# Performance work log

Measured on AMD Instinct MI355X. Metric: run time of the kernel, lower is better.

The kernel has to match this reference:

```python
import jax, jax.numpy as jnp
import numpy as np

EMBED_DIM = 256; N_HEADS = 8; HEAD_DIM = 32; N_PAIRS = 16
POS_DIM = 2; N_LEVELS = 4; NBH = [3, 5, 7, 9]
N_Q = 2048; BATCH = 2; FULL = 128
SPATIAL_THETA = 100.0; LEVEL_THETA = 10.0
LN_EPS = 1e-5


def _grids():
    offs, lvls = [], []
    for l, s in enumerate(NBH):
        ax = np.arange(s)
        g = np.stack(np.meshgrid(ax, ax, indexing='ij'), -1).reshape(-1, 2)
        offs.append(g - (s - 1) // 2)
        lvls.append(np.full(s * s, l))
    return (np.concatenate(offs).astype(np.int32), np.concatenate(lvls).astype(np.int32))

OFFSETS, LEVEL_IDS = _grids()  # [164,2], [164]
K_PER_Q = OFFSETS.shape[0]


def _apply_rope(x, pos, freqs):
    # x: [..., n_heads, n_pairs, 2]; pos: [..., 3]; freqs: [3, n_pairs]
    ang = pos @ freqs                      # [..., n_pairs]
    c = jnp.cos(ang)[..., None, :]         # broadcast over heads
    s = jnp.sin(ang)[..., None, :]
    x1, x2 = x[..., 0], x[..., 1]
    return jnp.stack([x1 * c - x2 * s, x1 * s + x2 * c], axis=-1)


def setup_inputs() -> dict:
    key = jax.random.key(0)
    ks = jax.random.split(key, 8)
    scale = EMBED_DIM ** -0.5
    i = jnp.arange(N_PAIRS, dtype=jnp.float32) / N_PAIRS
    rope_freqs = jnp.stack([SPATIAL_THETA ** -i, SPATIAL_THETA ** -i, LEVEL_THETA ** -i])  # [3,16]
    level_spatial_shapes = jnp.array([[FULL >> l, FULL >> l] for l in range(N_LEVELS)], jnp.int32)
    return {
        'query': jax.random.normal(ks[0], (N_Q, EMBED_DIM), jnp.float32),
        'query_spatial_positions': jax.random.uniform(ks[1], (N_Q, POS_DIM), jnp.float32) * (FULL - 1),
        'stacked_feature_maps': jax.random.normal(ks[2], (BATCH, N_LEVELS, FULL, FULL, EMBED_DIM), jnp.float32) * 0.02,
        'norm_w': jnp.ones((EMBED_DIM,), jnp.float32),
        'norm_b': jnp.zeros((EMBED_DIM,), jnp.float32),
        'q_w': jax.random.normal(ks[3], (EMBED_DIM, EMBED_DIM), jnp.float32) * scale,
        'k_w': jax.random.normal(ks[4], (EMBED_DIM, EMBED_DIM), jnp.float32) * scale,
        'v_w': jax.random.normal(ks[5], (EMBED_DIM, EMBED_DIM), jnp.float32) * scale,
        'out_w': jax.random.normal(ks[6], (EMBED_DIM, EMBED_DIM), jnp.float32) * scale,
        'rope_freqs': rope_freqs,
        'query_batch_offsets': jnp.array([0, N_Q // 2, N_Q], jnp.int32),
        'level_spatial_shapes': level_spatial_shapes,
    }


def reference(query, query_spatial_positions, stacked_feature_maps, norm_w, norm_b,
              q_w, k_w, v_w, out_w, rope_freqs, query_batch_offsets, level_spatial_shapes):
    n_q = query.shape[0]
    residual = query

    # pre-LayerNorm
    mu = query.mean(-1, keepdims=True)
    var = query.var(-1, keepdims=True)
    x = (query - mu) * jax.lax.rsqrt(var + LN_EPS) * norm_w + norm_b

    # query projection + RoPE (spatial dims + level dim; queries sit at max-res level 0)
    q = x @ q_w
    qpos = jnp.concatenate([query_spatial_positions, jnp.zeros((n_q, 1), query.dtype)], -1)  # [n_q,3]
    q_rot = _apply_rope(q.reshape(n_q, N_HEADS, N_PAIRS, 2), qpos, rope_freqs).reshape(n_q, N_HEADS, HEAD_DIM)

    # multilevel neighborhood indices
    shapes_f = level_spatial_shapes.astype(query.dtype)               # [L,2]
    scaling = shapes_f / shapes_f.max(0)                              # [L,2]
    scaled = query_spatial_positions[:, None, :] * scaling[None]      # [n_q,L,2]
    centers = jnp.floor(scaled).astype(jnp.int32)                     # [n_q,L,2]
    lvl = jnp.asarray(LEVEL_IDS)                                      # [K]
    idx = centers[:, lvl, :] + jnp.asarray(OFFSETS)[None]             # [n_q,K,2]
    lsh = level_spatial_shapes[lvl]                                   # [K,2]
    valid = jnp.all((idx >= 0) & (idx < lsh[None]), -1)               # [n_q,K]
    idxc = jnp.clip(idx, 0, lsh[None] - 1)

    # per-query batch ids from offsets
    b = jnp.searchsorted(query_batch_offsets, jnp.arange(n_q, dtype=query_batch_offsets.dtype), side='right') - 1

    # sparse gather of key/value features (unspecified -> zero)
    feats = stacked_feature_maps[b[:, None], lvl[None, :], idxc[..., 0], idxc[..., 1]]  # [n_q,K,E]
    feats = feats * valid[..., None].astype(feats.dtype)

    k = feats @ k_w
    v = feats @ v_w

    # key positions at full scale + level coordinate
    stride = (shapes_f.max(0)[None] / shapes_f)[lvl]                  # [K,2]
    kpos_sp = (idx.astype(query.dtype) + 0.5) * stride[None]          # [n_q,K,2]
    kpos = jnp.concatenate([kpos_sp, jnp.broadcast_to(lvl.astype(query.dtype), (n_q, K_PER_Q))[..., None]], -1)
    k_rot = _apply_rope(k.reshape(n_q, K_PER_Q, N_HEADS, N_PAIRS, 2), kpos, rope_freqs)
    k_rot = k_rot.reshape(n_q, K_PER_Q, N_HEADS, HEAD_DIM)

    # attention over the 164 gathered keys per query
    logits = jnp.einsum('nhd,nkhd->nhk', q_rot, k_rot) / np.sqrt(HEAD_DIM)
    logits = jnp.where(valid[:, None, :], logits, jnp.asarray(-1e9, logits.dtype))
    attn = jax.nn.softmax(logits, axis=-1)
    out = jnp.einsum('nhk,nkhd->nhd', attn, v.reshape(n_q, K_PER_Q, N_HEADS, HEAD_DIM))
    out = out.reshape(n_q, EMBED_DIM) @ out_w
    return out + residual
```

## Files before the change

### kernel.cpp

```cpp
#include <hip/hip_runtime.h>
#include <hip/hip_bf16.h>

typedef unsigned short u16;
typedef short short8 __attribute__((ext_vector_type(8)));
typedef float f32x4 __attribute__((ext_vector_type(4)));

#define ROWS_PER_BATCH 21760
#define TOT_ROWS 43520

__device__ __forceinline__ u16 f2bf(float f){
  unsigned u = __builtin_bit_cast(unsigned, f);
  u += 0x7FFFu + ((u >> 16) & 1u);
  return (u16)(u >> 16);
}
__device__ __forceinline__ float bf2f(u16 h){
  return __builtin_bit_cast(float, ((unsigned)h) << 16);
}
__device__ __forceinline__ float bflo(unsigned u){ return __builtin_bit_cast(float, u << 16); }
__device__ __forceinline__ float bfhi(unsigned u){ return __builtin_bit_cast(float, u & 0xFFFF0000u); }
__device__ __forceinline__ unsigned pk2bf(float a, float b){
  __hip_bfloat162 h = __float22bfloat162_rn(make_float2(a, b));
  union { __hip_bfloat162 h2; unsigned u; } cv; cv.h2 = h; return cv.u;
}

__global__ __launch_bounds__(256) void prep_kernel(
    const float* __restrict__ qw, const float* __restrict__ kw,
    const float* __restrict__ vw, const float* __restrict__ ow,
    const float* __restrict__ q, const float* __restrict__ nw,
    const float* __restrict__ nb,
    u16* __restrict__ wtq, u16* __restrict__ wtk,
    u16* __restrict__ wtv, u16* __restrict__ wto, u16* __restrict__ x){
  const int bx = blockIdx.x;
  const int t = threadIdx.x;
  if (bx < 128){
    int e = bx * 256 + t;
    int which = e >> 13;
    int r = e & 8191;
    int cg = r >> 9;
    int kk = (r >> 6) & 7;
    int lane = r & 63;
    int quad = lane >> 4, mn = lane & 15;
    const float* s = which == 0 ? qw : which == 1 ? kw : which == 2 ? vw : ow;
    u16* d       = which == 0 ? wtq : which == 1 ? wtk : which == 2 ? wtv : wto;
    const float* base = s + (kk * 32 + quad * 8) * 256 + cg * 16 + mn;
    float e8[8];
    #pragma unroll
    for (int j = 0; j < 8; ++j) e8[j] = base[j * 256];
    uint4 o = { pk2bf(e8[0], e8[1]), pk2bf(e8[2], e8[3]),
                pk2bf(e8[4], e8[5]), pk2bf(e8[6], e8[7]) };
    *(uint4*)(d + (size_t)r * 8) = o;
  } else {
    const int row = (bx - 128) * 4 + (t >> 6);
    const int lane = t & 63;
    const float4 v = *(const float4*)(q + (size_t)row * 256 + lane * 4);
    float s1 = v.x + v.y + v.z + v.w;
    float s2 = v.x*v.x + v.y*v.y + v.z*v.z + v.w*v.w;
    #pragma unroll
    for (int o = 32; o > 0; o >>= 1){
      s1 += __shfl_xor(s1, o);
      s2 += __shfl_xor(s2, o);
    }
    float mu = s1 * (1.0f / 256.0f);
    float var = s2 * (1.0f / 256.0f) - mu * mu;
    float rs = rsqrtf(var + 1e-5f);
    const float4 wv = *(const float4*)(nw + lane * 4);
    const float4 bv = *(const float4*)(nb + lane * 4);
    float o0 = (v.x - mu) * rs * wv.x + bv.x;
    float o1 = (v.y - mu) * rs * wv.y + bv.y;
    float o2 = (v.z - mu) * rs * wv.z + bv.z;
    float o3 = (v.w - mu) * rs * wv.w + bv.w;
    uint2 pk = { pk2bf(o0, o1), pk2bf(o2, o3) };
    *(uint2*)(x + (size_t)row * 256 + lane * 4) = pk;
  }
}

__global__ __launch_bounds__(256, 4) void kv_gemm(const float* __restrict__ fm,
        const u16* __restrict__ wtkp, const u16* __restrict__ wtvp,
        const float* __restrict__ rope,
        u16* __restrict__ krot, u16* __restrict__ vmap){
  __shared__ float slab[4][16][66];
  __shared__ unsigned sh_cs[4][16][16];

  const int t = threadIdx.x;
  const int row0 = blockIdx.x * 64;
  const int m = blockIdx.y;
  const u16* wtp = m ? wtvp : wtkp;
  u16* outp = m ? vmap : krot;

  const int b = row0 / ROWS_PER_BATCH;
  const int rr = row0 - b * ROWS_PER_BATCH;
  int l, loff;
  if (rr < 16384)      { l = 0; loff = 0; }
  else if (rr < 20480) { l = 1; loff = 16384; }
  else if (rr < 21504) { l = 2; loff = 20480; }
  else                 { l = 3; loff = 21504; }
  const int logW = 7 - l;
  const int Wm1 = (128 >> l) - 1;
  const int cell0 = rr - loff;
  const float* fmbase = fm + (size_t)(b * 4 + l) * (128 * 128 * 256);

  const int wv = t >> 6;
  const int lane = t & 63;
  const int mn = lane & 15;
  const int quad = lane >> 4;

  short8 af[8];
  {
    int cell = cell0 + wv * 16 + mn;
    int y = cell >> logW, x = cell & Wm1;
    const float* arow = fmbase + (((y << 7) + x) << 8) + quad * 8;
    #pragma unroll
    for (int kk = 0; kk < 8; ++kk){
      float4 a0 = *(const float4*)(arow + kk * 32);
      float4 a1 = *(const float4*)(arow + kk * 32 + 4);
      union { short8 s; uint4 u; } cv;
      cv.u = (uint4){ pk2bf(a0.x, a0.y), pk2bf(a0.z, a0.w),
                      pk2bf(a1.x, a1.y), pk2bf(a1.z, a1.w) };
      af[kk] = cv.s;
    }
  }

  if (m == 0){
    #pragma unroll
    for (int i = 0; i < 4; ++i){
      int id = i * 64 + lane;
      int lr = id >> 4, p = id & 15;
      int cell = cell0 + wv * 16 + lr;
      int i0 = cell >> logW;
      int i1 = cell & Wm1;
      float fs = (float)(1 << l);
      float kx = ((float)i0 + 0.5f) * fs;
      float ky = ((float)i1 + 0.5f) * fs;
      float ang = kx * rope[p] + ky * rope[16 + p] + (float)l * rope[32 + p];
      sh_cs[wv][lr][p] = pk2bf(__cosf(ang), __sinf(ang));
    }
  }

  for (int cs2 = 0; cs2 < 4; ++cs2){
    const u16* wb = wtp + (size_t)((cs2 * 4 * 8) * 64 + lane) * 8;
    short8 bc[4], bn[4];
    #pragma unroll
    for (int tl = 0; tl < 4; ++tl)
      bc[tl] = *(const short8*)(wb + (size_t)(tl * 8) * 64 * 8);
    f32x4 acc[4];
    #pragma unroll
    for (int i = 0; i < 4; ++i) acc[i] = (f32x4){0.f, 0.f, 0.f, 0.f};
    #pragma unroll
    for (int kk = 0; kk < 8; ++kk){
      if (kk < 7){
        #pragma unroll
        for (int tl = 0; tl < 4; ++tl)
          bn[tl] = *(const short8*)(wb + (size_t)(tl * 8 + kk + 1) * 64 * 8);
      }
      #pragma unroll
      for (int tl = 0; tl < 4; ++tl)
        acc[tl] = __builtin_amdgcn_mfma_f32_16x16x32_bf16(af[kk], bc[tl], acc[tl], 0, 0, 0);
      #pragma unroll
      for (int tl = 0; tl < 4; ++tl) bc[tl] = bn[tl];
    }
    #pragma unroll
    for (int tl = 0; tl < 4; ++tl)
      #pragma unroll
      for (int r = 0; r < 4; ++r)
        slab[wv][quad * 4 + r][tl * 16 + mn] = acc[tl][r];
    #pragma unroll
    for (int i = 0; i < 8; ++i){
      int pi = i * 64 + lane;
      int row = pi >> 5;
      int pl = pi & 31;
      float2 kv2 = *(const float2*)&slab[wv][row][pl * 2];
      unsigned o;
      if (m == 0){
        unsigned csn = sh_cs[wv][row][pl & 15];
        float c = bflo(csn), s = bfhi(csn);
        o = pk2bf(kv2.x * c - kv2.y * s, kv2.x * s + kv2.y * c);
      } else {
        o = pk2bf(kv2.x, kv2.y);
      }
      *(unsigned*)(outp + (size_t)(row0 + wv * 16 + row) * 256 + cs2 * 64 + pl * 2) = o;
    }
  }
}

__global__ __launch_bounds__(256) void gemm_xw(const u16* __restrict__ A,
        const u16* __restrict__ wt, const float* __restrict__ resid,
        float* __restrict__ out){
  const int t = threadIdx.x;
  const int row0 = blockIdx.x * 16;
  const int wv = t >> 6;
  const int lane = t & 63;
  const int mn = lane & 15;
  const int quad = lane >> 4;
  const int cg = blockIdx.y * 4 + wv;

  short8 af[8];
  {
    const u16* arow = A + (size_t)(row0 + mn) * 256 + quad * 8;
    #pragma unroll
    for (int kk = 0; kk < 8; ++kk)
      af[kk] = *(const short8*)(arow + kk * 32);
  }
  const u16* wb = wt + (size_t)((cg * 8) * 64 + lane) * 8;
  short8 bc = *(const short8*)wb;
  f32x4 acc = (f32x4){0.f, 0.f, 0.f, 0.f};
  #pragma unroll
  for (int kk = 0; kk < 8; ++kk){
    short8 bn;
    if (kk < 7) bn = *(const short8*)(wb + (size_t)(kk + 1) * 64 * 8);
    acc = __builtin_amdgcn_mfma_f32_16x16x32_bf16(af[kk], bc, acc, 0, 0, 0);
    bc = bn;
  }
  const int col = cg * 16 + mn;
  #pragma unroll
  for (int r = 0; r < 4; ++r){
    int row = row0 + quad * 4 + r;
    float val = acc[r];
    if (resid) val += resid[(size_t)row * 256 + col];
    out[(size_t)row * 256 + col] = val;
  }
}

__global__ __launch_bounds__(256) void attn2(
    const float* __restrict__ qraw, const float* __restrict__ qsp,
    const float* __restrict__ rope, const int* __restrict__ qbo, int nbo,
    const u16* __restrict__ krot, const u16* __restrict__ vmap,
    u16* __restrict__ ao){
  __shared__ float sh_q[8][33];
  __shared__ float sh_lg[8][168];
  __shared__ int   sh_row[176];
  __shared__ float sh_inv[8];
  __shared__ float sh_pv[2][128][2];
  const int t = threadIdx.x;
  const int qi = blockIdx.x;

  int bidx = 0;
  for (int j = 1; j < nbo; ++j) if (qi >= qbo[j]) bidx = j;
  const float p0 = qsp[qi * 2 + 0];
  const float p1 = qsp[qi * 2 + 1];

  {
    float qv = qraw[(size_t)qi * 256 + t];
    int p = (t & 31) >> 1;
    float ang = p0 * rope[p] + p1 * rope[16 + p];
    float c = __cosf(ang), s = __sinf(ang);
    float partner = __shfl_xor(qv, 1);
    float val = (t & 1) ? (partner * s + qv * c) : (qv * c - partner * s);
    sh_q[t >> 5][t & 31] = val * 0.17677669529663687f;
  }

  if (t < 164){
    int l, dy, dx, loff;
    if (t < 9)       { l = 0; int j = t;      dy = j / 3 - 1; dx = j % 3 - 1; loff = 0; }
    else if (t < 34) { l = 1; int j = t - 9;  dy = j / 5 - 2; dx = j % 5 - 2; loff = 16384; }
    else if (t < 83) { l = 2; int j = t - 34; dy = j / 7 - 3; dx = j % 7 - 3; loff = 20480; }
    else             { l = 3; int j = t - 83; dy = j / 9 - 4; dx = j % 9 - 4; loff = 21504; }
    float sc = 1.0f / (float)(1 << l);
    int i0 = (int)floorf(p0 * sc) + dy;
    int i1 = (int)floorf(p1 * sc) + dx;
    int W = 128 >> l;
    sh_row[t] = (i0 < 0 || i0 >= W || i1 < 0 || i1 >= W)
              ? -1 : bidx * ROWS_PER_BATCH + loff + (i0 << (7 - l)) + i1;
  }
  __syncthreads();

  const int h = t & 7;
  const int kbase = t >> 3;
  float qreg[32];
  #pragma unroll
  for (int d = 0; d < 32; ++d) qreg[d] = sh_q[h][d];
  for (int pass = 0; pass < 6; ++pass){
    int kk = pass * 32 + kbase;
    if (kk < 164){
      int row = sh_row[kk];
      float lg = -1e9f;
      if (row >= 0){
        const uint4* kp = (const uint4*)(krot + (size_t)row * 256 + h * 32);
        uint4 A0 = kp[0], A1 = kp[1], A2 = kp[2], A3 = kp[3];
        unsigned uu[16];
        uu[0]=A0.x; uu[1]=A0.y; uu[2]=A0.z; uu[3]=A0.w;
        uu[4]=A1.x; uu[5]=A1.y; uu[6]=A1.z; uu[7]=A1.w;
        uu[8]=A2.x; uu[9]=A2.y; uu[10]=A2.z; uu[11]=A2.w;
        uu[12]=A3.x; uu[13]=A3.y; uu[14]=A3.z; uu[15]=A3.w;
        lg = 0.f;
        #pragma unroll
        for (int j = 0; j < 16; ++j)
          lg += qreg[2*j] * bflo(uu[j]) + qreg[2*j+1] * bfhi(uu[j]);
      }
      sh_lg[h][kk] = lg;
    }
  }
  __syncthreads();

  const int h3 = t >> 5;
  const int l32 = t & 31;
  float mx = -1e30f;
  for (int kk = l32; kk < 164; kk += 32) mx = fmaxf(mx, sh_lg[h3][kk]);
  #pragma unroll
  for (int o = 16; o > 0; o >>= 1) mx = fmaxf(mx, __shfl_xor(mx, o));
  float ssum = 0.f;
  for (int kk = l32; kk < 164; kk += 32){
    float e = __expf(sh_lg[h3][kk] - mx);
    sh_lg[h3][kk] = e;
    ssum += e;
  }
  #pragma unroll
  for (int o = 16; o > 0; o >>= 1) ssum += __shfl_xor(ssum, o);
  if (l32 == 0) sh_inv[h3] = 1.0f / ssum;
  __syncthreads();

  {
    const int half = t >> 7;
    const int d2 = t & 127;
    const int hh = d2 >> 4;
    float a0 = 0.f, a1 = 0.f;
    const int k0 = half * 82;
    #pragma unroll 4
    for (int kk = k0; kk < k0 + 82; ++kk){
      int row = sh_row[kk];
      int rc = row < 0 ? 0 : row;
      unsigned vv = *(const unsigned*)(vmap + (size_t)rc * 256 + d2 * 2);
      float e = sh_lg[hh][kk];
      a0 += e * bflo(vv);
      a1 += e * bfhi(vv);
    }
    sh_pv[half][d2][0] = a0;
    sh_pv[half][d2][1] = a1;
  }
  __syncthreads();
  if (t < 128){
    const int hh = t >> 4;
    float inv = sh_inv[hh];
    float o0 = (sh_pv[0][t][0] + sh_pv[1][t][0]) * inv;
    float o1 = (sh_pv[0][t][1] + sh_pv[1][t][1]) * inv;
    *(unsigned*)(ao + (size_t)qi * 256 + t * 2) = pk2bf(o0, o1);
  }
}

extern "C" void kernel_launch(void* const* d_in, const int* in_sizes, int n_in,
                              void* d_out, int out_size, void* d_ws, size_t ws_size,
                              hipStream_t stream) {
  (void)n_in; (void)out_size; (void)ws_size;
  const float* query  = (const float*)d_in[0];
  const float* qsp    = (const float*)d_in[1];
  const float* fm     = (const float*)d_in[2];
  const float* norm_w = (const float*)d_in[3];
  const float* norm_b = (const float*)d_in[4];
  const float* q_w    = (const float*)d_in[5];
  const float* k_w    = (const float*)d_in[6];
  const float* v_w    = (const float*)d_in[7];
  const float* out_w  = (const float*)d_in[8];
  const float* rope   = (const float*)d_in[9];
  const int*   qbo    = (const int*)d_in[10];
  float* out = (float*)d_out;
  const int n_q = in_sizes[0] / 256;
  const int nbo = in_sizes[10];

  char* p = (char*)d_ws;
  u16* krot = (u16*)p;                       p += (size_t)TOT_ROWS * 256 * 2;
  u16* vmap = (u16*)p;                       p += (size_t)TOT_ROWS * 256 * 2;
  float* qraw = (float*)p;                   p += (size_t)n_q * 256 * 4;
  u16* xbf = (u16*)p;                        p += (size_t)n_q * 256 * 2;
  u16* wtq = (u16*)p;                        p += 65536 * 2;
  u16* wtk = (u16*)p;                        p += 65536 * 2;
  u16* wtv = (u16*)p;                        p += 65536 * 2;
  u16* wto = (u16*)p;
  u16* ao = xbf;

  hipLaunchKernelGGL(prep_kernel, dim3(128 + n_q / 4), dim3(256), 0, stream,
                     q_w, k_w, v_w, out_w, query, norm_w, norm_b,
                     wtq, wtk, wtv, wto, xbf);
  hipLaunchKernelGGL(kv_gemm, dim3(TOT_ROWS / 64, 2), dim3(256), 0, stream,
                     fm, wtk, wtv, rope, krot, vmap);
  hipLaunchKernelGGL(gemm_xw, dim3(n_q / 16, 4), dim3(256), 0, stream,
                     xbf, wtq, (const float*)nullptr, qraw);
  hipLaunchKernelGGL(attn2, dim3(n_q), dim3(256), 0, stream,
                     qraw, qsp, rope, qbo, nbo, krot, vmap, ao);
  hipLaunchKernelGGL(gemm_xw, dim3(n_q / 16, 4), dim3(256), 0, stream,
                     ao, wto, query, out);
}
```

Measured before the change: 281.2 us.

## Load feature tile once for K and V, one wavefront per query in attention

The KV projection now uses single-wavefront blocks of 16 rows, each computing both K and V from one register-resident bf16 A tile. Previously the fp32 feature map was read and converted twice, once per projection. The attention kernel maps one query to one wavefront (four per block), which removes block-wide __syncthreads and the split-half PV reduction. The trade-offs are smaller blocks and longer serial loops per wave, which may hurt latency hiding.

```diff
diff --git a/kernel.cpp b/kernel.cpp
--- a/kernel.cpp
+++ b/kernel.cpp
@@ -74,18 +74,15 @@
   }
 }
 
-__global__ __launch_bounds__(256, 4) void kv_gemm(const float* __restrict__ fm,
+__global__ __launch_bounds__(64, 4) void kv_gemm(const float* __restrict__ fm,
         const u16* __restrict__ wtkp, const u16* __restrict__ wtvp,
         const float* __restrict__ rope,
         u16* __restrict__ krot, u16* __restrict__ vmap){
-  __shared__ float slab[4][16][66];
-  __shared__ unsigned sh_cs[4][16][16];
-
-  const int t = threadIdx.x;
-  const int row0 = blockIdx.x * 64;
-  const int m = blockIdx.y;
-  const u16* wtp = m ? wtvp : wtkp;
-  u16* outp = m ? vmap : krot;
+  __shared__ float slab[16][66];
+  __shared__ unsigned sh_cs[16][16];
+
+  const int lane = threadIdx.x;
+  const int row0 = blockIdx.x * 16;
 
   const int b = row0 / ROWS_PER_BATCH;
   const int rr = row0 - b * ROWS_PER_BATCH;
@@ -99,14 +96,12 @@
   const int cell0 = rr - loff;
   const float* fmbase = fm + (size_t)(b * 4 + l) * (128 * 128 * 256);
 
-  const int wv = t >> 6;
-  const int lane = t & 63;
   const int mn = lane & 15;
   const int quad = lane >> 4;
 
   short8 af[8];
   {
-    int cell = cell0 + wv * 16 + mn;
+    int cell = cell0 + mn;
     int y = cell >> logW, x = cell & Wm1;
     const float* arow = fmbase + (((y << 7) + x) << 8) + quad * 8;
     #pragma unroll
@@ -120,64 +115,66 @@
     }
   }
 
-  if (m == 0){
-    #pragma unroll
-    for (int i = 0; i < 4; ++i){
-      int id = i * 64 + lane;
-      int lr = id >> 4, p = id & 15;
-      int cell = cell0 + wv * 16 + lr;
-      int i0 = cell >> logW;
-      int i1 = cell & Wm1;
-      float fs = (float)(1 << l);
-      float kx = ((float)i0 + 0.5f) * fs;
-      float ky = ((float)i1 + 0.5f) * fs;
-      float ang = kx * rope[p] + ky * rope[16 + p] + (float)l * rope[32 + p];
-      sh_cs[wv][lr][p] = pk2bf(__cosf(ang), __sinf(ang));
-    }
-  }
-
-  for (int cs2 = 0; cs2 < 4; ++cs2){
-    const u16* wb = wtp + (size_t)((cs2 * 4 * 8) * 64 + lane) * 8;
-    short8 bc[4], bn[4];
-    #pragma unroll
-    for (int tl = 0; tl < 4; ++tl)
-      bc[tl] = *(const short8*)(wb + (size_t)(tl * 8) * 64 * 8);
-    f32x4 acc[4];
-    #pragma unroll
-    for (int i = 0; i < 4; ++i) acc[i] = (f32x4){0.f, 0.f, 0.f, 0.f};
-    #pragma unroll
-    for (int kk = 0; kk < 8; ++kk){
-      if (kk < 7){
+  #pragma unroll
+  for (int i = 0; i < 4; ++i){
+    int id = i * 64 + lane;
+    int lr = id >> 4, p = id & 15;
+    int cell = cell0 + lr;
+    int i0 = cell >> logW;
+    int i1 = cell & Wm1;
+    float fs = (float)(1 << l);
+    float kx = ((float)i0 + 0.5f) * fs;
+    float ky = ((float)i1 + 0.5f) * fs;
+    float ang = kx * rope[p] + ky * rope[16 + p] + (float)l * rope[32 + p];
+    sh_cs[lr][p] = pk2bf(__cosf(ang), __sinf(ang));
+  }
+
+  for (int m = 0; m < 2; ++m){
+    const u16* wtp = m ? wtvp : wtkp;
+    u16* outp = m ? vmap : krot;
+    for (int cs2 = 0; cs2 < 4; ++cs2){
+      const u16* wb = wtp + (size_t)((cs2 * 4 * 8) * 64 + lane) * 8;
+      short8 bc[4], bn[4];
+      #pragma unroll
+      for (int tl = 0; tl < 4; ++tl)
+        bc[tl] = *(const short8*)(wb + (size_t)(tl * 8) * 64 * 8);
+      f32x4 acc[4];
+      #pragma unroll
+      for (int i = 0; i < 4; ++i) acc[i] = (f32x4){0.f, 0.f, 0.f, 0.f};
+      #pragma unroll
+      for (int kk = 0; kk < 8; ++kk){
+        if (kk < 7){
+          #pragma unroll
+          for (int tl = 0; tl < 4; ++tl)
+            bn[tl] = *(const short8*)(wb + (size_t)(tl * 8 + kk + 1) * 64 * 8);
+        }
         #pragma unroll
         for (int tl = 0; tl < 4; ++tl)
-          bn[tl] = *(const short8*)(wb + (size_t)(tl * 8 + kk + 1) * 64 * 8);
+          acc[tl] = __builtin_amdgcn_mfma_f32_16x16x32_bf16(af[kk], bc[tl], acc[tl], 0, 0, 0);
+        #pragma unroll
+        for (int tl = 0; tl < 4; ++tl) bc[tl] = bn[tl];
       }
       #pragma unroll
       for (int tl = 0; tl < 4; ++tl)
-        acc[tl] = __builtin_amdgcn_mfma_f32_16x16x32_bf16(af[kk], bc[tl], acc[tl], 0, 0, 0);
-      #pragma unroll
-      for (int tl = 0; tl < 4; ++tl) bc[tl] = bn[tl];
-    }
-    #pragma unroll
-    for (int tl = 0; tl < 4; ++tl)
-      #pragma unroll
-      for (int r = 0; r < 4; ++r)
-        slab[wv][quad * 4 + r][tl * 16 + mn] = acc[tl][r];
-    #pragma unroll
-    for (int i = 0; i < 8; ++i){
-      int pi = i * 64 + lane;
-      int row = pi >> 5;
-      int pl = pi & 31;
-      float2 kv2 = *(const float2*)&slab[wv][row][pl * 2];
-      unsigned o;
-      if (m == 0){
-        unsigned csn = sh_cs[wv][row][pl & 15];
-        float c = bflo(csn), s = bfhi(csn);
-        o = pk2bf(kv2.x * c - kv2.y * s, kv2.x * s + kv2.y * c);
-      } else {
-        o = pk2bf(kv2.x, kv2.y);
+        #pragma unroll
+        for (int r = 0; r < 4; ++r)
+          slab[quad * 4 + r][tl * 16 + mn] = acc[tl][r];
+      #pragma unroll
+      for (int i = 0; i < 8; ++i){
+        int pi = i * 64 + lane;
+        int row = pi >> 5;
+        int pl = pi & 31;
+        float2 kv2 = *(const float2*)&slab[row][pl * 2];
+        unsigned o;
+        if (m == 0){
+          unsigned csn = sh_cs[row][pl & 15];
+          float c = bflo(csn), s = bfhi(csn);
+          o = pk2bf(kv2.x * c - kv2.y * s, kv2.x * s + kv2.y * c);
+        } else {
+          o = pk2bf(kv2.x, kv2.y);
+        }
+        *(unsigned*)(outp + (size_t)(row0 + row) * 256 + cs2 * 64 + pl * 2) = o;
       }
-      *(unsigned*)(outp + (size_t)(row0 + wv * 16 + row) * 256 + cs2 * 64 + pl * 2) = o;
     }
   }
 }
@@ -220,58 +217,64 @@
   }
 }
 
-__global__ __launch_bounds__(256) void attn2(
+__global__ __launch_bounds__(256) void attn3(
     const float* __restrict__ qraw, const float* __restrict__ qsp,
     const float* __restrict__ rope, const int* __restrict__ qbo, int nbo,
     const u16* __restrict__ krot, const u16* __restrict__ vmap,
     u16* __restrict__ ao){
-  __shared__ float sh_q[8][33];
-  __shared__ float sh_lg[8][168];
-  __shared__ int   sh_row[176];
-  __shared__ float sh_inv[8];
-  __shared__ float sh_pv[2][128][2];
+  __shared__ float sh_q[4][8][33];
+  __shared__ float sh_lg[4][168][8];
+  __shared__ int   sh_row[4][168];
+  __shared__ float sh_inv[4][8];
   const int t = threadIdx.x;
-  const int qi = blockIdx.x;
+  const int w = t >> 6;
+  const int lane = t & 63;
+  const int qi = blockIdx.x * 4 + w;
 
   int bidx = 0;
   for (int j = 1; j < nbo; ++j) if (qi >= qbo[j]) bidx = j;
   const float p0 = qsp[qi * 2 + 0];
   const float p1 = qsp[qi * 2 + 1];
 
-  {
-    float qv = qraw[(size_t)qi * 256 + t];
-    int p = (t & 31) >> 1;
+  #pragma unroll
+  for (int it = 0; it < 4; ++it){
+    int d = it * 64 + lane;
+    float qv = qraw[(size_t)qi * 256 + d];
+    int p = (d & 31) >> 1;
     float ang = p0 * rope[p] + p1 * rope[16 + p];
     float c = __cosf(ang), s = __sinf(ang);
     float partner = __shfl_xor(qv, 1);
-    float val = (t & 1) ? (partner * s + qv * c) : (qv * c - partner * s);
-    sh_q[t >> 5][t & 31] = val * 0.17677669529663687f;
-  }
-
-  if (t < 164){
-    int l, dy, dx, loff;
-    if (t < 9)       { l = 0; int j = t;      dy = j / 3 - 1; dx = j % 3 - 1; loff = 0; }
-    else if (t < 34) { l = 1; int j = t - 9;  dy = j / 5 - 2; dx = j % 5 - 2; loff = 16384; }
-    else if (t < 83) { l = 2; int j = t - 34; dy = j / 7 - 3; dx = j % 7 - 3; loff = 20480; }
-    else             { l = 3; int j = t - 83; dy = j / 9 - 4; dx = j % 9 - 4; loff = 21504; }
-    float sc = 1.0f / (float)(1 << l);
-    int i0 = (int)floorf(p0 * sc) + dy;
-    int i1 = (int)floorf(p1 * sc) + dx;
-    int W = 128 >> l;
-    sh_row[t] = (i0 < 0 || i0 >= W || i1 < 0 || i1 >= W)
-              ? -1 : bidx * ROWS_PER_BATCH + loff + (i0 << (7 - l)) + i1;
-  }
-  __syncthreads();
-
-  const int h = t & 7;
-  const int kbase = t >> 3;
+    float val = (d & 1) ? (partner * s + qv * c) : (qv * c - partner * s);
+    sh_q[w][d >> 5][d & 31] = val * 0.17677669529663687f;
+  }
+
+  #pragma unroll
+  for (int it = 0; it < 3; ++it){
+    int kk = it * 64 + lane;
+    if (kk < 164){
+      int l, dy, dx, loff;
+      if (kk < 9)       { l = 0; int j = kk;      dy = j / 3 - 1; dx = j % 3 - 1; loff = 0; }
+      else if (kk < 34) { l = 1; int j = kk - 9;  dy = j / 5 - 2; dx = j % 5 - 2; loff = 16384; }
+      else if (kk < 83) { l = 2; int j = kk - 34; dy = j / 7 - 3; dx = j % 7 - 3; loff = 20480; }
+      else              { l = 3; int j = kk - 83; dy = j / 9 - 4; dx = j % 9 - 4; loff = 21504; }
+      float sc = 1.0f / (float)(1 << l);
+      int i0 = (int)floorf(p0 * sc) + dy;
+      int i1 = (int)floorf(p1 * sc) + dx;
+      int W = 128 >> l;
+      sh_row[w][kk] = (i0 < 0 || i0 >= W || i1 < 0 || i1 >= W)
+                ? -1 : bidx * ROWS_PER_BATCH + loff + (i0 << (7 - l)) + i1;
+    }
+  }
+
+  const int h = lane & 7;
+  const int ksub = lane >> 3;
   float qreg[32];
   #pragma unroll
-  for (int d = 0; d < 32; ++d) qreg[d] = sh_q[h][d];
-  for (int pass = 0; pass < 6; ++pass){
-    int kk = pass * 32 + kbase;
+  for (int j = 0; j < 32; ++j) qreg[j] = sh_q[w][h][j];
+  for (int pass = 0; pass < 21; ++pass){
+    int kk = pass * 8 + ksub;
     if (kk < 164){
-      int row = sh_row[kk];
+      int row = sh_row[w][kk];
       float lg = -1e9f;
       if (row >= 0){
         const uint4* kp = (const uint4*)(krot + (size_t)row * 256 + h * 32);
@@ -286,54 +289,40 @@
         for (int j = 0; j < 16; ++j)
           lg += qreg[2*j] * bflo(uu[j]) + qreg[2*j+1] * bfhi(uu[j]);
       }
-      sh_lg[h][kk] = lg;
-    }
-  }
-  __syncthreads();
-
-  const int h3 = t >> 5;
-  const int l32 = t & 31;
+      sh_lg[w][kk][h] = lg;
+    }
+  }
+
   float mx = -1e30f;
-  for (int kk = l32; kk < 164; kk += 32) mx = fmaxf(mx, sh_lg[h3][kk]);
-  #pragma unroll
-  for (int o = 16; o > 0; o >>= 1) mx = fmaxf(mx, __shfl_xor(mx, o));
+  for (int kk = ksub; kk < 164; kk += 8) mx = fmaxf(mx, sh_lg[w][kk][h]);
+  #pragma unroll
+  for (int o = 8; o < 64; o <<= 1) mx = fmaxf(mx, __shfl_xor(mx, o));
   float ssum = 0.f;
-  for (int kk = l32; kk < 164; kk += 32){
-    float e = __expf(sh_lg[h3][kk] - mx);
-    sh_lg[h3][kk] = e;
+  for (int kk = ksub; kk < 164; kk += 8){
+    float e = __expf(sh_lg[w][kk][h] - mx);
+    sh_lg[w][kk][h] = e;
     ssum += e;
   }
   #pragma unroll
-  for (int o = 16; o > 0; o >>= 1) ssum += __shfl_xor(ssum, o);
-  if (l32 == 0) sh_inv[h3] = 1.0f / ssum;
-  __syncthreads();
-
-  {
-    const int half = t >> 7;
-    const int d2 = t & 127;
-    const int hh = d2 >> 4;
-    float a0 = 0.f, a1 = 0.f;
-    const int k0 = half * 82;
-    #pragma unroll 4
-    for (int kk = k0; kk < k0 + 82; ++kk){
-      int row = sh_row[kk];
-      int rc = row < 0 ? 0 : row;
-      unsigned vv = *(const unsigned*)(vmap + (size_t)rc * 256 + d2 * 2);
-      float e = sh_lg[hh][kk];
-      a0 += e * bflo(vv);
-      a1 += e * bfhi(vv);
-    }
-    sh_pv[half][d2][0] = a0;
-    sh_pv[half][d2][1] = a1;
-  }
-  __syncthreads();
-  if (t < 128){
-    const int hh = t >> 4;
-    float inv = sh_inv[hh];
-    float o0 = (sh_pv[0][t][0] + sh_pv[1][t][0]) * inv;
-    float o1 = (sh_pv[0][t][1] + sh_pv[1][t][1]) * inv;
-    *(unsigned*)(ao + (size_t)qi * 256 + t * 2) = pk2bf(o0, o1);
-  }
+  for (int o = 8; o < 64; o <<= 1) ssum += __shfl_xor(ssum, o);
+  if (ksub == 0) sh_inv[w][h] = 1.0f / ssum;
+
+  const int hh = lane >> 3;
+  float a0 = 0.f, a1 = 0.f, a2 = 0.f, a3 = 0.f;
+  #pragma unroll 4
+  for (int kk = 0; kk < 164; ++kk){
+    int row = sh_row[w][kk];
+    int rc = row < 0 ? 0 : row;
+    uint2 vv = *(const uint2*)(vmap + (size_t)rc * 256 + lane * 4);
+    float e = sh_lg[w][kk][hh];
+    a0 += e * bflo(vv.x);
+    a1 += e * bfhi(vv.x);
+    a2 += e * bflo(vv.y);
+    a3 += e * bfhi(vv.y);
+  }
+  float inv = sh_inv[w][hh];
+  uint2 o = { pk2bf(a0 * inv, a1 * inv), pk2bf(a2 * inv, a3 * inv) };
+  *(uint2*)(ao + (size_t)qi * 256 + lane * 4) = o;
 }
 
 extern "C" void kernel_launch(void* const* d_in, const int* in_sizes, int n_in,
@@ -369,11 +358,11 @@
   hipLaunchKernelGGL(prep_kernel, dim3(128 + n_q / 4), dim3(256), 0, stream,
                      q_w, k_w, v_w, out_w, query, norm_w, norm_b,
                      wtq, wtk, wtv, wto, xbf);
-  hipLaunchKernelGGL(kv_gemm, dim3(TOT_ROWS / 64, 2), dim3(256), 0, stream,
+  hipLaunchKernelGGL(kv_gemm, dim3(TOT_ROWS / 16), dim3(64), 0, stream,
                      fm, wtk, wtv, rope, krot, vmap);
   hipLaunchKernelGGL(gemm_xw, dim3(n_q / 16, 4), dim3(256), 0, stream,
                      xbf, wtq, (const float*)nullptr, qraw);
-  hipLaunchKernelGGL(attn2, dim3(n_q), dim3(256), 0, stream,
+  hipLaunchKernelGGL(attn3, dim3(n_q / 4), dim3(256), 0, stream,
                      qraw, qsp, rope, qbo, nbo, krot, vmap, ao);
   hipLaunchKernelGGL(gemm_xw, dim3(n_q / 16, 4), dim3(256), 0, stream,
                      ao, wto, query, out);
```

Result: faster. 270.3 us (-3.9%).
